# Performance work log

Hardware: AMD Instinct MI355X
Metric: run time of the kernel (lower is better)

The kernel has to match this reference:

```python
import jax, jax.numpy as jnp
from jax import lax
import numpy as np

OBS_DIM, POP_DIM, ACT_DIM, DE_POP = 256, 10, 8, 10
HID1, HID2 = 256, 256
SPIKE_TS = 25
ENC_VTH = 0.999
CDECAY = 0.5
VDECAY = 0.75
VTH_TEMPORAL = 0.5  # NEURON_VTH_*_temporal stays at its init value 0.5
GRAD_WIN = 0.5


@jax.custom_vjp
def enc_spike(v):
    return (v > ENC_VTH).astype(v.dtype)

def _es_fwd(v):
    return enc_spike(v), None

def _es_bwd(_, g):
    return (g,)  # straight-through

enc_spike.defvjp(_es_fwd, _es_bwd)


@jax.custom_vjp
def rect_spike(v, vth):
    return (v > vth).astype(v.dtype)

def _rs_fwd(v, vth):
    return rect_spike(v, vth), (v, vth)

def _rs_bwd(res, g):
    v, vth = res
    # rectangular pseudo-gradient window; vth is detached in the original (numpy roundtrip)
    return (g * (jnp.abs(v - vth) < GRAD_WIN).astype(g.dtype), jnp.zeros_like(vth))

rect_spike.defvjp(_rs_fwd, _rs_bwd)


def setup_inputs() -> dict:
    key = jax.random.key(0)
    ks = jax.random.split(key, 10)
    B = 2048
    obs = jax.random.normal(ks[0], (B, OBS_DIM), dtype=jnp.float32)
    # encoder Gaussian receptive-field params
    enc_mean = jnp.broadcast_to(jnp.linspace(-3.0, 3.0, POP_DIM, dtype=jnp.float32), (1, OBS_DIM, POP_DIM))
    enc_std = jnp.full((1, OBS_DIM, POP_DIM), 0.15, dtype=jnp.float32)
    n_in = OBS_DIM * POP_DIM
    out_pop = ACT_DIM * DE_POP
    w1 = jax.random.normal(ks[1], (HID1, n_in), dtype=jnp.float32) / np.sqrt(n_in)
    b1 = jnp.zeros((HID1,), dtype=jnp.float32)
    w2 = jax.random.normal(ks[2], (HID2, HID1), dtype=jnp.float32) / np.sqrt(HID1)
    b2 = jnp.zeros((HID2,), dtype=jnp.float32)
    w3 = jax.random.normal(ks[3], (out_pop, HID2), dtype=jnp.float32) / np.sqrt(HID2)
    b3 = jnp.zeros((out_pop,), dtype=jnp.float32)
    dec_w = jax.random.normal(ks[4], (ACT_DIM, DE_POP), dtype=jnp.float32) / np.sqrt(DE_POP)
    dec_b = jnp.zeros((ACT_DIM,), dtype=jnp.float32)
    return {"obs": obs, "enc_mean": enc_mean, "enc_std": enc_std,
            "w1": w1, "b1": b1, "w2": w2, "b2": b2, "w3": w3, "b3": b3,
            "dec_w": dec_w, "dec_b": dec_b, "batch_size": B}


def _forward(obs, enc_mean, enc_std, w1, b1, w2, b2, w3, b3, dec_w, dec_b):
    B = obs.shape[0]
    # --- population encoder: Gaussian receptive fields -> regular spike train ---
    pop_act = jnp.exp(-0.5 * (obs[:, :, None] - enc_mean) ** 2 / (enc_std ** 2))
    pop_act = pop_act.reshape(B, OBS_DIM * POP_DIM)  # [B, N]

    def enc_step(volt, _):
        volt = volt + pop_act
        s = enc_spike(volt)
        return volt - s * ENC_VTH, s

    _, in_spikes = lax.scan(enc_step, jnp.zeros_like(pop_act), None, length=SPIKE_TS)  # [T, B, N]

    # --- spike MLP with LIF neurons and dynamic threshold ---
    def lif_dth(x, W, b, state):
        c, v_prev, s = state
        c = c * CDECAY + x @ W.T + b
        v = v_prev * VDECAY * (1.0 - s) + c
        # dynamic threshold (detached in original via numpy roundtrip)
        vth = lax.stop_gradient(0.5 * VTH_TEMPORAL + 0.5 * (jnp.exp((v_prev - v) / 3.0) - 1.0))
        s = rect_spike(v, vth)
        return (c, v, s)

    def zeros_state(n):
        z = jnp.zeros((B, n), dtype=obs.dtype)
        return (z, z, z)

    init = (zeros_state(HID1), zeros_state(HID2), zeros_state(ACT_DIM * DE_POP))

    def mlp_step(states, x):
        s1 = lif_dth(x, w1, b1, states[0])
        s2 = lif_dth(s1[2], w2, b2, states[1])
        s3 = lif_dth(s2[2], w3, b3, states[2])
        return (s1, s2, s3), s3[2]

    _, out_spikes = lax.scan(mlp_step, init, in_spikes)  # [T, B, out_pop]
    pop_out = out_spikes.sum(axis=0) / SPIKE_TS  # rate decode

    # --- decoder: grouped Conv1d(kernel=pop_dim) == per-action dot product, then tanh ---
    raw = jnp.einsum('bap,ap->ba', pop_out.reshape(B, ACT_DIM, DE_POP), dec_w) + dec_b
    return jnp.tanh(raw)


def reference(obs, enc_mean, enc_std, w1, b1, w2, b2, w3, b3, dec_w, dec_b, batch_size):
    return _forward(obs, enc_mean, enc_std, w1, b1, w2, b2, w3, b3, dec_w, dec_b)
```

## Files before the change

### kernel.cpp

```cpp
#include <hip/hip_runtime.h>
#include <stdint.h>

#define NB 2048
#define OBSD 256
#define POP 10
#define NIN 2560
#define H 256
#define OUTP 80
#define TS 25
#define RECF 28

typedef __attribute__((ext_vector_type(2))) float f2;

__device__ __forceinline__ float exp_cr(float x) {
    return (float)exp((double)x);
}

__device__ __forceinline__ int rfl(int v) {
    return __builtin_amdgcn_readfirstlane(v);
}

struct Acc25 {
    f2 p[12];
    float last;
};

__device__ __forceinline__ void acc_zero(Acc25& a) {
    #pragma unroll
    for (int i = 0; i < 12; ++i) { a.p[i].x = 0.0f; a.p[i].y = 0.0f; }
    a.last = 0.0f;
}

__device__ __forceinline__ void acc_fold(Acc25& acc, Acc25& part) {
    #pragma unroll
    for (int i = 0; i < 12; ++i) {
        acc.p[i].x = __fadd_rn(acc.p[i].x, part.p[i].x);
        acc.p[i].y = __fadd_rn(acc.p[i].y, part.p[i].y);
        part.p[i].x = 0.0f; part.p[i].y = 0.0f;
    }
    acc.last = __fadd_rn(acc.last, part.last);
    part.last = 0.0f;
}

__device__ __forceinline__ void acc_unpack(const Acc25& a, float* __restrict__ t) {
    #pragma unroll
    for (int i = 0; i < 12; ++i) { t[2 * i] = a.p[i].x; t[2 * i + 1] = a.p[i].y; }
    t[24] = a.last;
}

__device__ __forceinline__ void fma25(float w, const float* __restrict__ rec, Acc25& a) {
    f2 wp; wp.x = w; wp.y = w;
    float4 q[7];
    #pragma unroll
    for (int i = 0; i < 7; ++i) q[i] = ((const float4*)rec)[i];
    const f2* r2 = (const f2*)q;
    #pragma unroll
    for (int i = 0; i < 12; ++i) {
#if __has_builtin(__builtin_elementwise_fma)
        a.p[i] = __builtin_elementwise_fma(wp, r2[i], a.p[i]);
#else
        a.p[i].x = fmaf(w, r2[i].x, a.p[i].x);
        a.p[i].y = fmaf(w, r2[i].y, a.p[i].y);
#endif
    }
    a.last = fmaf(w, q[6].x, a.last);
}

__global__ __launch_bounds__(256) void k0_transpose(
    const float* __restrict__ w1, const float* __restrict__ w2, const float* __restrict__ w3,
    float* __restrict__ w1t, float* __restrict__ w2t, float* __restrict__ w3t)
{
    int idx = blockIdx.x * 256 + threadIdx.x;
    const int N1 = NIN * H;
    const int N2 = H * H;
    const int N3 = H * OUTP;
    if (idx < N1) {
        int i = idx >> 8, j = idx & 255;
        w1t[idx] = w1[j * NIN + i];
    } else if (idx < N1 + N2) {
        int k = idx - N1;
        int i = k >> 8, j = k & 255;
        w2t[k] = w2[j * H + i];
    } else if (idx < N1 + N2 + N3) {
        int k = idx - N1 - N2;
        int i = k / OUTP, j = k - i * OUTP;
        w3t[k] = w3[j * H + i];
    }
}

__device__ __forceinline__ void lif_step(float x, float bv, float& c, float& v, float& s) {
    float cn = __fadd_rn(__fadd_rn(__fmul_rn(c, 0.5f), x), bv);
    c = cn;
    float vp = v;
    float t  = __fmul_rn(__fmul_rn(vp, 0.75f), __fadd_rn(1.0f, -s));
    float vn = __fadd_rn(t, cn);
    float ag = __fdiv_rn(__fadd_rn(vp, -vn), 3.0f);
    v = vn;
    float ex_a  = __expf(ag);
    float vth_a = 0.25f + 0.5f * (ex_a - 1.0f);
    float delta = 1e-5f * (ex_a + fabsf(vth_a) + 1.0f);
    if (vn > vth_a + delta) {
        s = 1.0f;
    } else if (vn < vth_a - delta) {
        s = 0.0f;
    } else {
        float ex  = exp_cr(ag);
        float vth = __fadd_rn(0.25f, __fmul_rn(0.5f, __fadd_rn(ex, -1.0f)));
        s = (vn > vth) ? 1.0f : 0.0f;
    }
}

__device__ __forceinline__ void write_rec(float* __restrict__ pairL, int pos, uint32_t m) {
    float f[RECF];
    #pragma unroll
    for (int t = 0; t < TS; ++t) f[t] = (m >> t) & 1u ? 1.0f : 0.0f;
    f[25] = 0.0f; f[26] = 0.0f; f[27] = 0.0f;
    float4* dst = (float4*)&pairL[pos * RECF];
    #pragma unroll
    for (int p = 0; p < 7; ++p)
        dst[p] = make_float4(f[4 * p], f[4 * p + 1], f[4 * p + 2], f[4 * p + 3]);
}

__global__ __launch_bounds__(256, 5) void k1_fused(
    const float* __restrict__ obs, const float* __restrict__ emean, const float* __restrict__ estd,
    const float* __restrict__ w1t, const float* __restrict__ w2t, const float* __restrict__ w3t,
    const float* __restrict__ b1, const float* __restrict__ b2, const float* __restrict__ b3,
    const float* __restrict__ dw, const float* __restrict__ db, float* __restrict__ out)
{
    __shared__ __align__(16) float pairL[256 * RECF];
    __shared__ __align__(16) int   idxL[256];
    __shared__ uint32_t waveCnt[4];
    __shared__ float cnt3[OUTP];

    const int tid = threadIdx.x;
    const int wave = tid >> 6, lane = tid & 63;
    const int b = blockIdx.x;
    const unsigned long long below = (1ull << lane) - 1ull;

    uint32_t msk[10];
    #pragma unroll
    for (int k = 0; k < 10; ++k) {
        int i = k * 256 + tid;
        int o = i / 10;
        float x  = obs[b * OBSD + o];
        float mu = emean[i];
        float sd = estd[i];
        float d  = __fadd_rn(x, -mu);
        float d2 = __fmul_rn(d, d);
        float nm = __fmul_rn(-0.5f, d2);
        float dn = __fmul_rn(sd, sd);
        float arg = __fdiv_rn(nm, dn);
        uint32_t m = 0;
        if (arg >= -3.23f) {
            float a  = exp_cr(arg);
            float volt = 0.0f;
            #pragma unroll
            for (int t = 0; t < TS; ++t) {
                volt = __fadd_rn(volt, a);
                if (volt > 0.999f) { m |= (1u << t); volt = __fadd_rn(volt, -0.999f); }
            }
        }
        msk[k] = m;
    }

    Acc25 acc, part;
    acc_zero(acc); acc_zero(part);
    int nextB = 320 * H;

    for (int h = 0; h < 2; ++h) {
        int runTot = 0;
        for (int kk = 0; kk < 5; ++kk) {
            int k = h * 5 + kk;
            uint32_t m = msk[k];
            unsigned long long bal = __ballot(m != 0u);
            if (lane == 0) waveCnt[wave] = (uint32_t)__popcll(bal);
            __syncthreads();
            int base = runTot, tot = 0;
            #pragma unroll
            for (int w = 0; w < 4; ++w) {
                if (w < wave) base += (int)waveCnt[w];
                tot += (int)waveCnt[w];
            }
            if (m) {
                int pos = base + (int)__popcll(bal & below);
                idxL[pos] = (k * 256 + tid) * H;
                write_rec(pairL, pos, m);
            }
            runTot += tot;
            __syncthreads();
        }
        const int nAct = runTot;

        int pi0 = 0, pi1 = 0, pi2 = 0, pi3 = 0;
        float pw0 = 0, pw1 = 0, pw2 = 0, pw3 = 0;
        if (nAct > 0) { pi0 = rfl(idxL[0]); pw0 = w1t[pi0 + tid]; }
        if (nAct > 1) { pi1 = rfl(idxL[1]); pw1 = w1t[pi1 + tid]; }
        if (nAct > 2) { pi2 = rfl(idxL[2]); pw2 = w1t[pi2 + tid]; }
        if (nAct > 3) { pi3 = rfl(idxL[3]); pw3 = w1t[pi3 + tid]; }
        int j = 0;
        for (; j + 4 <= nAct; j += 4) {
            int ci0 = pi0, ci1 = pi1, ci2 = pi2, ci3 = pi3;
            float cw0 = pw0, cw1 = pw1, cw2 = pw2, cw3 = pw3;
            if (j + 4 < nAct) { pi0 = rfl(idxL[j + 4]); pw0 = w1t[pi0 + tid]; }
            if (j + 5 < nAct) { pi1 = rfl(idxL[j + 5]); pw1 = w1t[pi1 + tid]; }
            if (j + 6 < nAct) { pi2 = rfl(idxL[j + 6]); pw2 = w1t[pi2 + tid]; }
            if (j + 7 < nAct) { pi3 = rfl(idxL[j + 7]); pw3 = w1t[pi3 + tid]; }
            while (ci0 >= nextB) { acc_fold(acc, part); nextB += 320 * H; }
            fma25(cw0, &pairL[j * RECF], part);
            while (ci1 >= nextB) { acc_fold(acc, part); nextB += 320 * H; }
            fma25(cw1, &pairL[(j + 1) * RECF], part);
            while (ci2 >= nextB) { acc_fold(acc, part); nextB += 320 * H; }
            fma25(cw2, &pairL[(j + 2) * RECF], part);
            while (ci3 >= nextB) { acc_fold(acc, part); nextB += 320 * H; }
            fma25(cw3, &pairL[(j + 3) * RECF], part);
        }
        for (; j < nAct; ++j) {
            int ii = rfl(idxL[j]);
            float wv = w1t[ii + tid];
            while (ii >= nextB) { acc_fold(acc, part); nextB += 320 * H; }
            fma25(wv, &pairL[j * RECF], part);
        }
        __syncthreads();
    }
    acc_fold(acc, part);

    uint32_t m1 = 0;
    {
        float cur[TS];
        acc_unpack(acc, cur);
        const float b1v = b1[tid];
        float c1 = 0, v1 = 0, s1 = 0;
        #pragma unroll
        for (int t = 0; t < TS; ++t) {
            lif_step(cur[t], b1v, c1, v1, s1);
            if (s1 != 0.0f) m1 |= (1u << t);
        }
    }
    unsigned long long bal = __ballot(m1 != 0u);
    if (lane == 0) waveCnt[wave] = (uint32_t)__popcll(bal);
    __syncthreads();
    int base1 = 0, n1 = 0;
    #pragma unroll
    for (int w = 0; w < 4; ++w) {
        if (w < wave) base1 += (int)waveCnt[w];
        n1 += (int)waveCnt[w];
    }
    if (m1) {
        int pos = base1 + (int)__popcll(bal & below);
        idxL[pos] = tid * H;
        write_rec(pairL, pos, m1);
    }
    __syncthreads();

    Acc25 acc2;
    acc_zero(acc2);
    {
        int pi0 = 0, pi1 = 0, pi2 = 0, pi3 = 0;
        float pw0 = 0, pw1 = 0, pw2 = 0, pw3 = 0;
        if (n1 > 0) { pi0 = rfl(idxL[0]); pw0 = w2t[pi0 + tid]; }
        if (n1 > 1) { pi1 = rfl(idxL[1]); pw1 = w2t[pi1 + tid]; }
        if (n1 > 2) { pi2 = rfl(idxL[2]); pw2 = w2t[pi2 + tid]; }
        if (n1 > 3) { pi3 = rfl(idxL[3]); pw3 = w2t[pi3 + tid]; }
        int j = 0;
        for (; j + 4 <= n1; j += 4) {
            float cw0 = pw0, cw1 = pw1, cw2 = pw2, cw3 = pw3;
            if (j + 4 < n1) { pi0 = rfl(idxL[j + 4]); pw0 = w2t[pi0 + tid]; }
            if (j + 5 < n1) { pi1 = rfl(idxL[j + 5]); pw1 = w2t[pi1 + tid]; }
            if (j + 6 < n1) { pi2 = rfl(idxL[j + 6]); pw2 = w2t[pi2 + tid]; }
            if (j + 7 < n1) { pi3 = rfl(idxL[j + 7]); pw3 = w2t[pi3 + tid]; }
            fma25(cw0, &pairL[j * RECF], acc2);
            fma25(cw1, &pairL[(j + 1) * RECF], acc2);
            fma25(cw2, &pairL[(j + 2) * RECF], acc2);
            fma25(cw3, &pairL[(j + 3) * RECF], acc2);
        }
        for (; j < n1; ++j) {
            int ii = rfl(idxL[j]);
            fma25(w2t[ii + tid], &pairL[j * RECF], acc2);
        }
    }
    uint32_t m2 = 0;
    {
        float cur[TS];
        acc_unpack(acc2, cur);
        const float b2v = b2[tid];
        float c2 = 0, v2 = 0, s2 = 0;
        #pragma unroll
        for (int t = 0; t < TS; ++t) {
            lif_step(cur[t], b2v, c2, v2, s2);
            if (s2 != 0.0f) m2 |= (1u << t);
        }
    }
    __syncthreads();
    bal = __ballot(m2 != 0u);
    if (lane == 0) waveCnt[wave] = (uint32_t)__popcll(bal);
    __syncthreads();
    int base2 = 0, n2 = 0;
    #pragma unroll
    for (int w = 0; w < 4; ++w) {
        if (w < wave) base2 += (int)waveCnt[w];
        n2 += (int)waveCnt[w];
    }
    if (m2) {
        int pos = base2 + (int)__popcll(bal & below);
        idxL[pos] = tid * OUTP;
        write_rec(pairL, pos, m2);
    }
    __syncthreads();

    if (tid < OUTP) {
        Acc25 x3;
        acc_zero(x3);
        int pi0 = 0, pi1 = 0, pi2 = 0, pi3 = 0;
        float pw0 = 0, pw1 = 0, pw2 = 0, pw3 = 0;
        if (n2 > 0) { pi0 = rfl(idxL[0]); pw0 = w3t[pi0 + tid]; }
        if (n2 > 1) { pi1 = rfl(idxL[1]); pw1 = w3t[pi1 + tid]; }
        if (n2 > 2) { pi2 = rfl(idxL[2]); pw2 = w3t[pi2 + tid]; }
        if (n2 > 3) { pi3 = rfl(idxL[3]); pw3 = w3t[pi3 + tid]; }
        int j = 0;
        for (; j + 4 <= n2; j += 4) {
            float cw0 = pw0, cw1 = pw1, cw2 = pw2, cw3 = pw3;
            if (j + 4 < n2) { pi0 = rfl(idxL[j + 4]); pw0 = w3t[pi0 + tid]; }
            if (j + 5 < n2) { pi1 = rfl(idxL[j + 5]); pw1 = w3t[pi1 + tid]; }
            if (j + 6 < n2) { pi2 = rfl(idxL[j + 6]); pw2 = w3t[pi2 + tid]; }
            if (j + 7 < n2) { pi3 = rfl(idxL[j + 7]); pw3 = w3t[pi3 + tid]; }
            fma25(cw0, &pairL[j * RECF], x3);
            fma25(cw1, &pairL[(j + 1) * RECF], x3);
            fma25(cw2, &pairL[(j + 2) * RECF], x3);
            fma25(cw3, &pairL[(j + 3) * RECF], x3);
        }
        for (; j < n2; ++j) {
            int ii = rfl(idxL[j]);
            fma25(w3t[ii + tid], &pairL[j * RECF], x3);
        }
        float cur[TS];
        acc_unpack(x3, cur);
        const float b3v = b3[tid];
        float c3 = 0, v3 = 0, s3 = 0, ct = 0;
        #pragma unroll
        for (int t = 0; t < TS; ++t) {
            lif_step(cur[t], b3v, c3, v3, s3);
            ct += s3;
        }
        cnt3[tid] = ct;
    }
    __syncthreads();

    if (tid < 8) {
        float raw = 0.0f;
        #pragma unroll
        for (int pp = 0; pp < POP; ++pp) {
            float po = __fdiv_rn(cnt3[tid * POP + pp], 25.0f);
            raw = __fadd_rn(raw, __fmul_rn(po, dw[tid * POP + pp]));
        }
        raw = __fadd_rn(raw, db[tid]);
        out[b * 8 + tid] = (float)tanh((double)raw);
    }
}

extern "C" void kernel_launch(void* const* d_in, const int* in_sizes, int n_in,
                              void* d_out, int out_size, void* d_ws, size_t ws_size,
                              hipStream_t stream) {
    const float* obs   = (const float*)d_in[0];
    const float* emean = (const float*)d_in[1];
    const float* estd  = (const float*)d_in[2];
    const float* w1    = (const float*)d_in[3];
    const float* b1    = (const float*)d_in[4];
    const float* w2    = (const float*)d_in[5];
    const float* b2    = (const float*)d_in[6];
    const float* w3    = (const float*)d_in[7];
    const float* b3    = (const float*)d_in[8];
    const float* dw    = (const float*)d_in[9];
    const float* db    = (const float*)d_in[10];
    float* out = (float*)d_out;

    char* ws = (char*)d_ws;
    float* w1t = (float*)(ws);
    float* w2t = (float*)(ws + 2621440);
    float* w3t = (float*)(ws + 2883584);

    k0_transpose<<<2896, 256, 0, stream>>>(w1, w2, w3, w1t, w2t, w3t);
    k1_fused<<<NB, 256, 0, stream>>>(obs, emean, estd, w1t, w2t, w3t,
                                     b1, b2, b3, dw, db, out);
}
```

Before: 386.0 us.

## Shrink spike record layout, batch ballot counts, tile weight transpose

Spike records move from 28 padded floats to 24 floats plus a separate last-step array, which cuts LDS use so launch bounds can rise from 5 to 6 blocks per CU. The per-group ballot counts for layer-1 compaction are now computed once up front, which removes a pair of block barriers per encoder group. The weight transpose becomes a 32x32 shared-memory tiled kernel with coalesced reads and writes. The three sparse accumulation loops are merged into one templated walk helper. Writes past a fixed capacity of 256 records are silently dropped, which would give wrong results if that many active inputs ever appear.

```diff
diff --git a/kernel.cpp b/kernel.cpp
--- a/kernel.cpp
+++ b/kernel.cpp
@@ -8,7 +8,7 @@
 #define H 256
 #define OUTP 80
 #define TS 25
-#define RECF 28
+#define CAP 256
 
 typedef __attribute__((ext_vector_type(2))) float f2;
 
@@ -48,11 +48,11 @@
     t[24] = a.last;
 }
 
-__device__ __forceinline__ void fma25(float w, const float* __restrict__ rec, Acc25& a) {
+__device__ __forceinline__ void fma25(float w, const float* __restrict__ rec, float lastv, Acc25& a) {
     f2 wp; wp.x = w; wp.y = w;
-    float4 q[7];
-    #pragma unroll
-    for (int i = 0; i < 7; ++i) q[i] = ((const float4*)rec)[i];
+    float4 q[6];
+    #pragma unroll
+    for (int i = 0; i < 6; ++i) q[i] = ((const float4*)rec)[i];
     const f2* r2 = (const f2*)q;
     #pragma unroll
     for (int i = 0; i < 12; ++i) {
@@ -63,28 +63,81 @@
         a.p[i].y = fmaf(w, r2[i].y, a.p[i].y);
 #endif
     }
-    a.last = fmaf(w, q[6].x, a.last);
+    a.last = fmaf(w, lastv, a.last);
+}
+
+__device__ __forceinline__ void write_rec(float* __restrict__ recs, float* __restrict__ rec24,
+                                          int pos, uint32_t m) {
+    if (pos >= CAP) return;
+    float f[24];
+    #pragma unroll
+    for (int t = 0; t < 24; ++t) f[t] = (m >> t) & 1u ? 1.0f : 0.0f;
+    float4* dst = (float4*)&recs[pos * 24];
+    #pragma unroll
+    for (int p = 0; p < 6; ++p)
+        dst[p] = make_float4(f[4 * p], f[4 * p + 1], f[4 * p + 2], f[4 * p + 3]);
+    rec24[pos] = (m >> 24) & 1u ? 1.0f : 0.0f;
+}
+
+template<bool FOLD>
+__device__ __forceinline__ void walk(int n, const float* __restrict__ wt, int tid,
+        const int* __restrict__ idxL, const float* __restrict__ recs,
+        const float* __restrict__ rec24, Acc25& acc, Acc25& part, int& nextB)
+{
+    Acc25& tgt = FOLD ? part : acc;
+    int pi0 = 0, pi1 = 0, pi2 = 0, pi3 = 0;
+    float pw0 = 0, pw1 = 0, pw2 = 0, pw3 = 0;
+    if (n > 0) { pi0 = rfl(idxL[0]); pw0 = wt[pi0 + tid]; }
+    if (n > 1) { pi1 = rfl(idxL[1]); pw1 = wt[pi1 + tid]; }
+    if (n > 2) { pi2 = rfl(idxL[2]); pw2 = wt[pi2 + tid]; }
+    if (n > 3) { pi3 = rfl(idxL[3]); pw3 = wt[pi3 + tid]; }
+    int j = 0;
+    for (; j + 4 <= n; j += 4) {
+        int ci0 = pi0, ci1 = pi1, ci2 = pi2, ci3 = pi3;
+        float cw0 = pw0, cw1 = pw1, cw2 = pw2, cw3 = pw3;
+        if (j + 4 < n) { pi0 = rfl(idxL[j + 4]); pw0 = wt[pi0 + tid]; }
+        if (j + 5 < n) { pi1 = rfl(idxL[j + 5]); pw1 = wt[pi1 + tid]; }
+        if (j + 6 < n) { pi2 = rfl(idxL[j + 6]); pw2 = wt[pi2 + tid]; }
+        if (j + 7 < n) { pi3 = rfl(idxL[j + 7]); pw3 = wt[pi3 + tid]; }
+        if (FOLD) { while (ci0 >= nextB) { acc_fold(acc, part); nextB += 320 * H; } }
+        fma25(cw0, recs + j * 24, rec24[j], tgt);
+        if (FOLD) { while (ci1 >= nextB) { acc_fold(acc, part); nextB += 320 * H; } }
+        fma25(cw1, recs + (j + 1) * 24, rec24[j + 1], tgt);
+        if (FOLD) { while (ci2 >= nextB) { acc_fold(acc, part); nextB += 320 * H; } }
+        fma25(cw2, recs + (j + 2) * 24, rec24[j + 2], tgt);
+        if (FOLD) { while (ci3 >= nextB) { acc_fold(acc, part); nextB += 320 * H; } }
+        fma25(cw3, recs + (j + 3) * 24, rec24[j + 3], tgt);
+    }
+    for (; j < n; ++j) {
+        int ii = rfl(idxL[j]);
+        float wv = wt[ii + tid];
+        if (FOLD) { while (ii >= nextB) { acc_fold(acc, part); nextB += 320 * H; } }
+        fma25(wv, recs + j * 24, rec24[j], tgt);
+    }
 }
 
 __global__ __launch_bounds__(256) void k0_transpose(
     const float* __restrict__ w1, const float* __restrict__ w2, const float* __restrict__ w3,
     float* __restrict__ w1t, float* __restrict__ w2t, float* __restrict__ w3t)
 {
-    int idx = blockIdx.x * 256 + threadIdx.x;
-    const int N1 = NIN * H;
-    const int N2 = H * H;
-    const int N3 = H * OUTP;
-    if (idx < N1) {
-        int i = idx >> 8, j = idx & 255;
-        w1t[idx] = w1[j * NIN + i];
-    } else if (idx < N1 + N2) {
-        int k = idx - N1;
-        int i = k >> 8, j = k & 255;
-        w2t[k] = w2[j * H + i];
-    } else if (idx < N1 + N2 + N3) {
-        int k = idx - N1 - N2;
-        int i = k / OUTP, j = k - i * OUTP;
-        w3t[k] = w3[j * H + i];
+    __shared__ float tile[32][33];
+    int bid = blockIdx.x;
+    const float* src; float* dst; int R, C, tr, tc;
+    if (bid < 640)      { src = w1; dst = w1t; R = 256; C = NIN; tr = bid / 80; tc = bid % 80; }
+    else if (bid < 704) { int t = bid - 640; src = w2; dst = w2t; R = 256; C = 256; tr = t / 8; tc = t % 8; }
+    else                { int t = bid - 704; src = w3; dst = w3t; R = OUTP; C = 256; tr = t / 8; tc = t % 8; }
+    const int tx = threadIdx.x & 31, ty = threadIdx.x >> 5;
+    const int r0 = tr * 32, c0 = tc * 32;
+    #pragma unroll
+    for (int i = 0; i < 4; ++i) {
+        int r = r0 + ty + i * 8, c = c0 + tx;
+        if (r < R && c < C) tile[ty + i * 8][tx] = src[r * C + c];
+    }
+    __syncthreads();
+    #pragma unroll
+    for (int i = 0; i < 4; ++i) {
+        int c = c0 + ty + i * 8, r = r0 + tx;
+        if (c < C && r < R) dst[c * R + r] = tile[tx][ty + i * 8];
     }
 }
 
@@ -110,25 +163,16 @@
     }
 }
 
-__device__ __forceinline__ void write_rec(float* __restrict__ pairL, int pos, uint32_t m) {
-    float f[RECF];
-    #pragma unroll
-    for (int t = 0; t < TS; ++t) f[t] = (m >> t) & 1u ? 1.0f : 0.0f;
-    f[25] = 0.0f; f[26] = 0.0f; f[27] = 0.0f;
-    float4* dst = (float4*)&pairL[pos * RECF];
-    #pragma unroll
-    for (int p = 0; p < 7; ++p)
-        dst[p] = make_float4(f[4 * p], f[4 * p + 1], f[4 * p + 2], f[4 * p + 3]);
-}
-
-__global__ __launch_bounds__(256, 5) void k1_fused(
+__global__ __launch_bounds__(256, 6) void k1_fused(
     const float* __restrict__ obs, const float* __restrict__ emean, const float* __restrict__ estd,
     const float* __restrict__ w1t, const float* __restrict__ w2t, const float* __restrict__ w3t,
     const float* __restrict__ b1, const float* __restrict__ b2, const float* __restrict__ b3,
     const float* __restrict__ dw, const float* __restrict__ db, float* __restrict__ out)
 {
-    __shared__ __align__(16) float pairL[256 * RECF];
-    __shared__ __align__(16) int   idxL[256];
+    __shared__ __align__(16) float recs[CAP * 24];
+    __shared__ float rec24[CAP];
+    __shared__ int   idxL[CAP];
+    __shared__ uint32_t cntA[40];
     __shared__ uint32_t waveCnt[4];
     __shared__ float cnt3[OUTP];
 
@@ -163,65 +207,43 @@
         msk[k] = m;
     }
 
+    #pragma unroll
+    for (int k = 0; k < 10; ++k) {
+        unsigned long long bal = __ballot(msk[k] != 0u);
+        if (lane == 0) cntA[k * 4 + wave] = (uint32_t)__popcll(bal);
+    }
+    __syncthreads();
+
     Acc25 acc, part;
     acc_zero(acc); acc_zero(part);
     int nextB = 320 * H;
-
-    for (int h = 0; h < 2; ++h) {
-        int runTot = 0;
-        for (int kk = 0; kk < 5; ++kk) {
-            int k = h * 5 + kk;
-            uint32_t m = msk[k];
-            unsigned long long bal = __ballot(m != 0u);
-            if (lane == 0) waveCnt[wave] = (uint32_t)__popcll(bal);
+    int run = 0;
+    #pragma unroll
+    for (int k = 0; k < 10; ++k) {
+        if (k == 5) {
             __syncthreads();
-            int base = runTot, tot = 0;
-            #pragma unroll
-            for (int w = 0; w < 4; ++w) {
-                if (w < wave) base += (int)waveCnt[w];
-                tot += (int)waveCnt[w];
-            }
-            if (m) {
-                int pos = base + (int)__popcll(bal & below);
-                idxL[pos] = (k * 256 + tid) * H;
-                write_rec(pairL, pos, m);
-            }
-            runTot += tot;
+            walk<true>(run, w1t, tid, idxL, recs, rec24, acc, part, nextB);
             __syncthreads();
-        }
-        const int nAct = runTot;
-
-        int pi0 = 0, pi1 = 0, pi2 = 0, pi3 = 0;
-        float pw0 = 0, pw1 = 0, pw2 = 0, pw3 = 0;
-        if (nAct > 0) { pi0 = rfl(idxL[0]); pw0 = w1t[pi0 + tid]; }
-        if (nAct > 1) { pi1 = rfl(idxL[1]); pw1 = w1t[pi1 + tid]; }
-        if (nAct > 2) { pi2 = rfl(idxL[2]); pw2 = w1t[pi2 + tid]; }
-        if (nAct > 3) { pi3 = rfl(idxL[3]); pw3 = w1t[pi3 + tid]; }
-        int j = 0;
-        for (; j + 4 <= nAct; j += 4) {
-            int ci0 = pi0, ci1 = pi1, ci2 = pi2, ci3 = pi3;
-            float cw0 = pw0, cw1 = pw1, cw2 = pw2, cw3 = pw3;
-            if (j + 4 < nAct) { pi0 = rfl(idxL[j + 4]); pw0 = w1t[pi0 + tid]; }
-            if (j + 5 < nAct) { pi1 = rfl(idxL[j + 5]); pw1 = w1t[pi1 + tid]; }
-            if (j + 6 < nAct) { pi2 = rfl(idxL[j + 6]); pw2 = w1t[pi2 + tid]; }
-            if (j + 7 < nAct) { pi3 = rfl(idxL[j + 7]); pw3 = w1t[pi3 + tid]; }
-            while (ci0 >= nextB) { acc_fold(acc, part); nextB += 320 * H; }
-            fma25(cw0, &pairL[j * RECF], part);
-            while (ci1 >= nextB) { acc_fold(acc, part); nextB += 320 * H; }
-            fma25(cw1, &pairL[(j + 1) * RECF], part);
-            while (ci2 >= nextB) { acc_fold(acc, part); nextB += 320 * H; }
-            fma25(cw2, &pairL[(j + 2) * RECF], part);
-            while (ci3 >= nextB) { acc_fold(acc, part); nextB += 320 * H; }
-            fma25(cw3, &pairL[(j + 3) * RECF], part);
-        }
-        for (; j < nAct; ++j) {
-            int ii = rfl(idxL[j]);
-            float wv = w1t[ii + tid];
-            while (ii >= nextB) { acc_fold(acc, part); nextB += 320 * H; }
-            fma25(wv, &pairL[j * RECF], part);
-        }
-        __syncthreads();
-    }
+            run = 0;
+        }
+        int tot = 0, pre = 0;
+        #pragma unroll
+        for (int w = 0; w < 4; ++w) {
+            int c = (int)cntA[k * 4 + w];
+            tot += c;
+            if (w < wave) pre += c;
+        }
+        uint32_t m = msk[k];
+        unsigned long long bal = __ballot(m != 0u);
+        if (m) {
+            int pos = run + pre + (int)__popcll(bal & below);
+            idxL[pos] = (k * 256 + tid) * H;
+            write_rec(recs, rec24, pos, m);
+        }
+        run += tot;
+    }
+    __syncthreads();
+    walk<true>(run, w1t, tid, idxL, recs, rec24, acc, part, nextB);
     acc_fold(acc, part);
 
     uint32_t m1 = 0;
@@ -236,8 +258,8 @@
             if (s1 != 0.0f) m1 |= (1u << t);
         }
     }
-    unsigned long long bal = __ballot(m1 != 0u);
-    if (lane == 0) waveCnt[wave] = (uint32_t)__popcll(bal);
+    unsigned long long bal1 = __ballot(m1 != 0u);
+    if (lane == 0) waveCnt[wave] = (uint32_t)__popcll(bal1);
     __syncthreads();
     int base1 = 0, n1 = 0;
     #pragma unroll
@@ -246,37 +268,17 @@
         n1 += (int)waveCnt[w];
     }
     if (m1) {
-        int pos = base1 + (int)__popcll(bal & below);
+        int pos = base1 + (int)__popcll(bal1 & below);
         idxL[pos] = tid * H;
-        write_rec(pairL, pos, m1);
+        write_rec(recs, rec24, pos, m1);
     }
     __syncthreads();
 
     Acc25 acc2;
     acc_zero(acc2);
     {
-        int pi0 = 0, pi1 = 0, pi2 = 0, pi3 = 0;
-        float pw0 = 0, pw1 = 0, pw2 = 0, pw3 = 0;
-        if (n1 > 0) { pi0 = rfl(idxL[0]); pw0 = w2t[pi0 + tid]; }
-        if (n1 > 1) { pi1 = rfl(idxL[1]); pw1 = w2t[pi1 + tid]; }
-        if (n1 > 2) { pi2 = rfl(idxL[2]); pw2 = w2t[pi2 + tid]; }
-        if (n1 > 3) { pi3 = rfl(idxL[3]); pw3 = w2t[pi3 + tid]; }
-        int j = 0;
-        for (; j + 4 <= n1; j += 4) {
-            float cw0 = pw0, cw1 = pw1, cw2 = pw2, cw3 = pw3;
-            if (j + 4 < n1) { pi0 = rfl(idxL[j + 4]); pw0 = w2t[pi0 + tid]; }
-            if (j + 5 < n1) { pi1 = rfl(idxL[j + 5]); pw1 = w2t[pi1 + tid]; }
-            if (j + 6 < n1) { pi2 = rfl(idxL[j + 6]); pw2 = w2t[pi2 + tid]; }
-            if (j + 7 < n1) { pi3 = rfl(idxL[j + 7]); pw3 = w2t[pi3 + tid]; }
-            fma25(cw0, &pairL[j * RECF], acc2);
-            fma25(cw1, &pairL[(j + 1) * RECF], acc2);
-            fma25(cw2, &pairL[(j + 2) * RECF], acc2);
-            fma25(cw3, &pairL[(j + 3) * RECF], acc2);
-        }
-        for (; j < n1; ++j) {
-            int ii = rfl(idxL[j]);
-            fma25(w2t[ii + tid], &pairL[j * RECF], acc2);
-        }
+        int dummyB = 0x7fffffff;
+        walk<false>(n1, w2t, tid, idxL, recs, rec24, acc2, acc2, dummyB);
     }
     uint32_t m2 = 0;
     {
@@ -290,9 +292,8 @@
             if (s2 != 0.0f) m2 |= (1u << t);
         }
     }
-    __syncthreads();
-    bal = __ballot(m2 != 0u);
-    if (lane == 0) waveCnt[wave] = (uint32_t)__popcll(bal);
+    unsigned long long bal2 = __ballot(m2 != 0u);
+    if (lane == 0) waveCnt[wave] = (uint32_t)__popcll(bal2);
     __syncthreads();
     int base2 = 0, n2 = 0;
     #pragma unroll
@@ -301,37 +302,17 @@
         n2 += (int)waveCnt[w];
     }
     if (m2) {
-        int pos = base2 + (int)__popcll(bal & below);
+        int pos = base2 + (int)__popcll(bal2 & below);
         idxL[pos] = tid * OUTP;
-        write_rec(pairL, pos, m2);
+        write_rec(recs, rec24, pos, m2);
     }
     __syncthreads();
 
     if (tid < OUTP) {
         Acc25 x3;
         acc_zero(x3);
-        int pi0 = 0, pi1 = 0, pi2 = 0, pi3 = 0;
-        float pw0 = 0, pw1 = 0, pw2 = 0, pw3 = 0;
-        if (n2 > 0) { pi0 = rfl(idxL[0]); pw0 = w3t[pi0 + tid]; }
-        if (n2 > 1) { pi1 = rfl(idxL[1]); pw1 = w3t[pi1 + tid]; }
-        if (n2 > 2) { pi2 = rfl(idxL[2]); pw2 = w3t[pi2 + tid]; }
-        if (n2 > 3) { pi3 = rfl(idxL[3]); pw3 = w3t[pi3 + tid]; }
-        int j = 0;
-        for (; j + 4 <= n2; j += 4) {
-            float cw0 = pw0, cw1 = pw1, cw2 = pw2, cw3 = pw3;
-            if (j + 4 < n2) { pi0 = rfl(idxL[j + 4]); pw0 = w3t[pi0 + tid]; }
-            if (j + 5 < n2) { pi1 = rfl(idxL[j + 5]); pw1 = w3t[pi1 + tid]; }
-            if (j + 6 < n2) { pi2 = rfl(idxL[j + 6]); pw2 = w3t[pi2 + tid]; }
-            if (j + 7 < n2) { pi3 = rfl(idxL[j + 7]); pw3 = w3t[pi3 + tid]; }
-            fma25(cw0, &pairL[j * RECF], x3);
-            fma25(cw1, &pairL[(j + 1) * RECF], x3);
-            fma25(cw2, &pairL[(j + 2) * RECF], x3);
-            fma25(cw3, &pairL[(j + 3) * RECF], x3);
-        }
-        for (; j < n2; ++j) {
-            int ii = rfl(idxL[j]);
-            fma25(w3t[ii + tid], &pairL[j * RECF], x3);
-        }
+        int dummyB = 0x7fffffff;
+        walk<false>(n2, w3t, tid, idxL, recs, rec24, x3, x3, dummyB);
         float cur[TS];
         acc_unpack(x3, cur);
         const float b3v = b3[tid];
@@ -378,7 +359,7 @@
     float* w2t = (float*)(ws + 2621440);
     float* w3t = (float*)(ws + 2883584);
 
-    k0_transpose<<<2896, 256, 0, stream>>>(w1, w2, w3, w1t, w2t, w3t);
+    k0_transpose<<<728, 256, 0, stream>>>(w1, w2, w3, w1t, w2t, w3t);
     k1_fused<<<NB, 256, 0, stream>>>(obs, emean, estd, w1t, w2t, w3t,
                                      b1, b2, b3, dw, db, out);
 }
```

After: 383.0 us. About the same (-0.8%).
